# Kernel optimization log

Measured on AMD Instinct MI355X. Metric: run time of the kernel, lower is better.

The kernel has to match this reference:

```python
import jax, jax.numpy as jnp
import numpy as np

NUM_GRIDS = 8
GRID_MIN, GRID_MAX = -2.0, 2.0
DENOM = (GRID_MAX - GRID_MIN) / (NUM_GRIDS - 1)
GRID = jnp.linspace(GRID_MIN, GRID_MAX, NUM_GRIDS, dtype=jnp.float32)

Q_DIM = K_DIM = V_DIM = 256
HEAD_DIM, NUM_HEADS = 32, 8
TOTAL = HEAD_DIM * NUM_HEADS  # 256
B, S = 128, 8192


def fastkan(x, spline_w, base_w, base_b):
    # RBF expansion: [N, in, G] (layernorm in original is built but never applied)
    basis = jnp.exp(-(((x[..., None] - GRID) / DENOM) ** 2))
    ret = basis.reshape(x.shape[0], -1) @ spline_w          # [N, out]
    base = jax.nn.silu(x) @ base_w + base_b                 # [N, out]
    return ret + base


def setup_inputs() -> dict:
    key = jax.random.key(0)
    ks = jax.random.split(key, 20)
    d = {
        "q": jax.random.normal(ks[0], (B, Q_DIM), jnp.float32),
        "k": jax.random.normal(ks[1], (S, K_DIM), jnp.float32),
        "v": jax.random.normal(ks[2], (S, V_DIM), jnp.float32),
    }
    i = 3
    for name, din, dout in (("q", Q_DIM, TOTAL), ("k", K_DIM, TOTAL), ("v", V_DIM, TOTAL), ("g", Q_DIM, TOTAL), ("o", TOTAL, Q_DIM)):
        d[f"{name}_sw"] = jax.random.truncated_normal(ks[i], -2.0, 2.0, (din * NUM_GRIDS, dout), jnp.float32) * 0.1
        d[f"{name}_bw"] = jax.random.normal(ks[i + 1], (din, dout), jnp.float32) * (1.0 / np.sqrt(din))
        d[f"{name}_bb"] = jnp.zeros((dout,), jnp.float32)
        i += 2
    return d


def reference(q, k, v,
              q_sw, q_bw, q_bb,
              k_sw, k_bw, k_bb,
              v_sw, v_bw, v_bb,
              g_sw, g_bw, g_bb,
              o_sw, o_bw, o_bb):
    norm = 1.0 / np.sqrt(HEAD_DIM)
    wq = (fastkan(q, q_sw, q_bw, q_bb) * norm).reshape(B, NUM_HEADS, HEAD_DIM)   # [B,H,D]
    wk = fastkan(k, k_sw, k_bw, k_bb).reshape(S, NUM_HEADS, HEAD_DIM)            # [S,H,D]
    # broadcast-multiply + reduce == einsum; softmax over key axis S
    att = jax.nn.softmax(jnp.einsum("bhd,shd->bsh", wq, wk), axis=1)             # [B,S,H]
    wv = fastkan(v, v_sw, v_bw, v_bb).reshape(S, NUM_HEADS, HEAD_DIM)            # [S,H,D]
    o = jnp.einsum("bsh,shd->bhd", att, wv).reshape(B, TOTAL)                    # [B,H*D]
    g = jax.nn.sigmoid(fastkan(q, g_sw, g_bw, g_bb))                             # [B,H*D]
    o = g * o
    return fastkan(o, o_sw, o_bw, o_bb)                                          # [B,q_dim]
```

## Files before the change

kernel.cpp:

```cpp
#include <hip/hip_runtime.h>
#include <math.h>

#define IN_DIM 256
#define OUT_DIM 256

typedef short short8 __attribute__((ext_vector_type(8)));
typedef short short4_t __attribute__((ext_vector_type(4)));
typedef float f32x4 __attribute__((ext_vector_type(4)));
typedef unsigned int u32;

static __device__ __forceinline__ short f2bf(float f) {
    union { float f; unsigned u; } c; c.f = f;
    unsigned r = (c.u + 0x7FFFu + ((c.u >> 16) & 1u)) >> 16;
    return (short)r;
}
static __device__ __forceinline__ float bf2f(short s) {
    union { unsigned u; float f; } c;
    c.u = ((u32)(unsigned short)s) << 16;
    return c.f;
}

static __device__ __forceinline__ void gload16(const void* g, void* l) {
    __builtin_amdgcn_global_load_lds(
        (const __attribute__((address_space(1))) u32*)g,
        (__attribute__((address_space(3))) u32*)l, 16, 0, 0);
}

template<int RT, int CT, int MODE>
__global__ __launch_bounds__(256) void fastkan_kernel(
    const float* __restrict__ X, const float* __restrict__ SW,
    const float* __restrict__ BW, const float* __restrict__ BB,
    float* __restrict__ OUT)
{
    constexpr int TRT = RT / 16;
    constexpr int TCT = CT / 16;
    __shared__ float aT[64][RT];
    __shared__ float bT[64][CT];
    const int t = threadIdx.x, tr = t >> 4, tc = t & 15;
    const int r0 = blockIdx.x * RT, c0 = blockIdx.y * CT;
    float acc[TRT][TCT];
#pragma unroll
    for (int a = 0; a < TRT; ++a)
#pragma unroll
        for (int b = 0; b < TCT; ++b) acc[a][b] = 0.f;

    for (int i0 = 0; i0 < IN_DIM; i0 += 8) {
        __syncthreads();
        constexpr int PER_A = (RT * 8) / 256;
#pragma unroll
        for (int j = 0; j < PER_A; ++j) {
            int p = j * 256 + t;
            int i = p & 7, r = p >> 3;
            float x = X[(size_t)(r0 + r) * IN_DIM + (i0 + i)];
#pragma unroll
            for (int g = 0; g < 8; ++g) {
                float z = (x - (-2.0f + (float)g * (4.0f / 7.0f))) * 1.75f;
                aT[i * 8 + g][r] = __expf(-z * z);
            }
        }
#pragma unroll
        for (int j = 0; j < (64 * CT) / 1024; ++j) {
            int p = j * 256 + t;
            int c4 = p % (CT / 4), kk = p / (CT / 4);
            *(float4*)&bT[kk][c4 * 4] =
                *(const float4*)&SW[(size_t)(i0 * 8 + kk) * OUT_DIM + (c0 + c4 * 4)];
        }
        __syncthreads();
#pragma unroll 8
        for (int kk = 0; kk < 64; ++kk) {
            float av[TRT], bv[TCT];
#pragma unroll
            for (int a = 0; a < TRT; ++a) av[a] = aT[kk][tr * TRT + a];
#pragma unroll
            for (int b = 0; b < TCT; ++b) bv[b] = bT[kk][tc * TCT + b];
#pragma unroll
            for (int a = 0; a < TRT; ++a)
#pragma unroll
                for (int b = 0; b < TCT; ++b)
                    acc[a][b] = fmaf(av[a], bv[b], acc[a][b]);
        }
    }
    for (int i0 = 0; i0 < IN_DIM; i0 += 64) {
        __syncthreads();
#pragma unroll
        for (int j = 0; j < (RT * 64) / 1024; ++j) {
            int p = j * 256 + t;
            int i4 = p & 15, r = p >> 4;
            float4 xv = *(const float4*)&X[(size_t)(r0 + r) * IN_DIM + (i0 + i4 * 4)];
            const float* xe = &xv.x;
#pragma unroll
            for (int e = 0; e < 4; ++e) {
                float x = xe[e];
                aT[i4 * 4 + e][r] = x / (1.f + __expf(-x));
            }
        }
#pragma unroll
        for (int j = 0; j < (64 * CT) / 1024; ++j) {
            int p = j * 256 + t;
            int c4 = p % (CT / 4), kk = p / (CT / 4);
            *(float4*)&bT[kk][c4 * 4] =
                *(const float4*)&BW[(size_t)(i0 + kk) * OUT_DIM + (c0 + c4 * 4)];
        }
        __syncthreads();
#pragma unroll 8
        for (int kk = 0; kk < 64; ++kk) {
            float av[TRT], bv[TCT];
#pragma unroll
            for (int a = 0; a < TRT; ++a) av[a] = aT[kk][tr * TRT + a];
#pragma unroll
            for (int b = 0; b < TCT; ++b) bv[b] = bT[kk][tc * TCT + b];
#pragma unroll
            for (int a = 0; a < TRT; ++a)
#pragma unroll
                for (int b = 0; b < TCT; ++b)
                    acc[a][b] = fmaf(av[a], bv[b], acc[a][b]);
        }
    }
#pragma unroll
    for (int a = 0; a < TRT; ++a) {
        int r = r0 + tr * TRT + a;
#pragma unroll
        for (int b = 0; b < TCT; ++b) {
            int c = c0 + tc * TCT + b;
            float v = acc[a][b] + BB[c];
            if (MODE == 1) v *= 0.17677669529663687f;
            if (MODE == 2) v = 1.f / (1.f + __expf(-v));
            OUT[(size_t)r * OUT_DIM + c] = v;
        }
    }
}

__global__ __launch_bounds__(256) void fastkan_splitk(
    const float* __restrict__ X,
    const float* __restrict__ SW0, const float* __restrict__ BW0,
    const float* __restrict__ SW1, const float* __restrict__ BW1,
    float* __restrict__ PART)
{
    __shared__ float aT[128][65];
    __shared__ float bT[64][33];

    const int t = threadIdx.x;
    const int tr = t >> 4, tc = t & 15;
    const int c0 = blockIdx.x * 32;
    const int kc = blockIdx.y;
    const int z = blockIdx.z;
    const float* SW = z ? SW1 : SW0;
    const float* BW = z ? BW1 : BW0;

    float acc[8][2];
#pragma unroll
    for (int a = 0; a < 8; ++a) { acc[a][0] = 0.f; acc[a][1] = 0.f; }

    for (int sub = 0; sub < 4; ++sub) {
        const int k0 = kc * 256 + sub * 64;
        __syncthreads();
        if (kc < 8) {
            const int i0 = kc * 32 + sub * 8;
#pragma unroll
            for (int it = 0; it < 4; ++it) {
                int p = it * 256 + t;
                int row = p & 127, i = p >> 7;
                float x = X[(size_t)row * 256 + i0 + i];
#pragma unroll
                for (int g = 0; g < 8; ++g) {
                    float zz = (x - (-2.0f + (float)g * (4.0f / 7.0f))) * 1.75f;
                    aT[row][i * 8 + g] = __expf(-zz * zz);
                }
            }
        } else {
            const int f0 = sub * 64;
            int row = t >> 1, seg = t & 1;
            const float* xr = &X[(size_t)row * 256 + f0 + seg * 32];
#pragma unroll
            for (int j4 = 0; j4 < 8; ++j4) {
                float4 xv = *(const float4*)&xr[j4 * 4];
                const float* xe = &xv.x;
#pragma unroll
                for (int e = 0; e < 4; ++e) {
                    float x = xe[e];
                    aT[row][seg * 32 + j4 * 4 + e] = x / (1.f + __expf(-x));
                }
            }
        }
        {
            const float* Wsrc = (kc < 8) ? &SW[(size_t)k0 * 256] : &BW[(size_t)(k0 - 2048) * 256];
#pragma unroll
            for (int it = 0; it < 2; ++it) {
                int p = it * 256 + t;
                int kk = p >> 3, c4 = p & 7;
                float4 v = *(const float4*)&Wsrc[(size_t)kk * 256 + c0 + c4 * 4];
                bT[kk][c4 * 4 + 0] = v.x; bT[kk][c4 * 4 + 1] = v.y;
                bT[kk][c4 * 4 + 2] = v.z; bT[kk][c4 * 4 + 3] = v.w;
            }
        }
        __syncthreads();
#pragma unroll 8
        for (int kk = 0; kk < 64; ++kk) {
            float av[8], bv[2];
#pragma unroll
            for (int a = 0; a < 8; ++a) av[a] = aT[tr * 8 + a][kk];
            bv[0] = bT[kk][tc * 2 + 0];
            bv[1] = bT[kk][tc * 2 + 1];
#pragma unroll
            for (int a = 0; a < 8; ++a) {
                acc[a][0] = fmaf(av[a], bv[0], acc[a][0]);
                acc[a][1] = fmaf(av[a], bv[1], acc[a][1]);
            }
        }
    }
#pragma unroll
    for (int a = 0; a < 8; ++a) {
        int r = tr * 8 + a;
        float* dst = &PART[((size_t)(z * 9 + kc) * 128 + r) * 256 + c0 + tc * 2];
        dst[0] = acc[a][0];
        dst[1] = acc[a][1];
    }
}

template<int MODE>
__global__ __launch_bounds__(256) void reduce_kernel(
    const float* __restrict__ PART, const float* __restrict__ BB, float* __restrict__ OUT)
{
    const int r = blockIdx.x, t = threadIdx.x;
    float s = 0.f;
#pragma unroll
    for (int kc = 0; kc < 9; ++kc)
        s += PART[((size_t)kc * 128 + r) * 256 + t];
    float v = s + BB[t];
    if (MODE == 1) v *= 0.17677669529663687f;
    if (MODE == 2) v = 1.f / (1.f + __expf(-v));
    OUT[(size_t)r * 256 + t] = v;
}

template<int WB>
__global__ __launch_bounds__(256) void reduce_qg(
    const float* __restrict__ PART, const float* __restrict__ QBB,
    const float* __restrict__ GBB, float* __restrict__ WQ, float* __restrict__ GB,
    short* __restrict__ WQb)
{
    const int r = blockIdx.x, t = threadIdx.x, z = blockIdx.y;
    const float* P = PART + (size_t)z * 9 * 128 * 256;
    float s = 0.f;
#pragma unroll
    for (int kc = 0; kc < 9; ++kc)
        s += P[((size_t)kc * 128 + r) * 256 + t];
    if (z == 0) {
        float v = (s + QBB[t]) * 0.17677669529663687f;
        WQ[(size_t)r * 256 + t] = v;
        if (WB) WQb[(size_t)r * 256 + t] = f2bf(v);
    } else {
        float v = s + GBB[t];
        GB[(size_t)r * 256 + t] = 1.f / (1.f + __expf(-v));
    }
}

__global__ __launch_bounds__(256) void prep_kernel(
    const float* __restrict__ SWk, const float* __restrict__ BWk, short* __restrict__ Bk,
    const float* __restrict__ SWv, const float* __restrict__ BWv, short* __restrict__ Bv)
{
    __shared__ float tile[64][65];
    const int t = threadIdx.x;
    const int kk0 = blockIdx.x * 64;
    const int c0 = blockIdx.y * 64;
    const float* SW = blockIdx.z ? SWv : SWk;
    const float* BW = blockIdx.z ? BWv : BWk;
    short* Bdst = blockIdx.z ? Bv : Bk;

#pragma unroll
    for (int j = 0; j < 4; ++j) {
        int p = j * 256 + t;
        int lr = p >> 4, lc4 = p & 15;
        float4 v;
        if (kk0 < 2048) v = *(const float4*)&SW[(size_t)(kk0 + lr) * 256 + c0 + lc4 * 4];
        else            v = *(const float4*)&BW[(size_t)(kk0 - 2048 + lr) * 256 + c0 + lc4 * 4];
        tile[lr][lc4 * 4 + 0] = v.x; tile[lr][lc4 * 4 + 1] = v.y;
        tile[lr][lc4 * 4 + 2] = v.z; tile[lr][lc4 * 4 + 3] = v.w;
    }
    __syncthreads();
#pragma unroll
    for (int j = 0; j < 4; ++j) {
        int p = j * 256 + t;
        int lc = p >> 4, lk4 = p & 15;
        short4_t s;
#pragma unroll
        for (int e = 0; e < 4; ++e) s[e] = f2bf(tile[lk4 * 4 + e][lc]);
        *(short4_t*)&Bdst[(size_t)(c0 + lc) * 2304 + kk0 + lk4 * 4] = s;
    }
}

__global__ __launch_bounds__(256) void basis_gen2(
    const float* __restrict__ K, const float* __restrict__ V,
    short* __restrict__ A0, short* __restrict__ A1)
{
    const float* X = blockIdx.y ? V : K;
    short* A = blockIdx.y ? A1 : A0;
    const int row = blockIdx.x;
    const int t = threadIdx.x;
    float x = X[(size_t)row * 256 + t];
    short8 s;
#pragma unroll
    for (int g = 0; g < 8; ++g) {
        float z = (x - (-2.0f + (float)g * (4.0f / 7.0f))) * 1.75f;
        s[g] = f2bf(__expf(-z * z));
    }
    *(short8*)&A[(size_t)row * 2304 + t * 8] = s;
    if (t < 32) {
        const float* xr = &X[(size_t)row * 256 + t * 8];
        short8 sl;
#pragma unroll
        for (int e2 = 0; e2 < 2; ++e2) {
            float4 xv = *(const float4*)&xr[e2 * 4];
            const float* xe = &xv.x;
#pragma unroll
            for (int e = 0; e < 4; ++e) {
                float xx = xe[e];
                sl[e2 * 4 + e] = f2bf(xx / (1.f + __expf(-xx)));
            }
        }
        *(short8*)&A[(size_t)row * 2304 + 2048 + t * 8] = sl;
    }
}

__global__ __launch_bounds__(256) void prep_basis(
    const float* __restrict__ K, const float* __restrict__ V,
    short* __restrict__ A0, short* __restrict__ A1,
    const float* __restrict__ SWk, const float* __restrict__ BWk, short* __restrict__ Bk,
    const float* __restrict__ SWv, const float* __restrict__ BWv, short* __restrict__ Bv)
{
    __shared__ float tile[64][65];
    const int bid = blockIdx.x;
    const int t = threadIdx.x;
    if (bid < 16384) {
        const float* X = (bid >> 13) ? V : K;
        short* A = (bid >> 13) ? A1 : A0;
        const int row = bid & 8191;
        float x = X[(size_t)row * 256 + t];
        short8 s;
#pragma unroll
        for (int g = 0; g < 8; ++g) {
            float z = (x - (-2.0f + (float)g * (4.0f / 7.0f))) * 1.75f;
            s[g] = f2bf(__expf(-z * z));
        }
        *(short8*)&A[(size_t)row * 2304 + t * 8] = s;
        if (t < 32) {
            const float* xr = &X[(size_t)row * 256 + t * 8];
            short8 sl;
#pragma unroll
            for (int e2 = 0; e2 < 2; ++e2) {
                float4 xv = *(const float4*)&xr[e2 * 4];
                const float* xe = &xv.x;
#pragma unroll
                for (int e = 0; e < 4; ++e) {
                    float xx = xe[e];
                    sl[e2 * 4 + e] = f2bf(xx / (1.f + __expf(-xx)));
                }
            }
            *(short8*)&A[(size_t)row * 2304 + 2048 + t * 8] = sl;
        }
        return;
    }
    const int p = bid - 16384;
    const int zz = p / 144;
    const int q = p % 144;
    const int kk0 = (q >> 2) * 64;
    const int c0 = (q & 3) * 64;
    const float* SW = zz ? SWv : SWk;
    const float* BW = zz ? BWv : BWk;
    short* Bdst = zz ? Bv : Bk;

#pragma unroll
    for (int j = 0; j < 4; ++j) {
        int pp = j * 256 + t;
        int lr = pp >> 4, lc4 = pp & 15;
        float4 v;
        if (kk0 < 2048) v = *(const float4*)&SW[(size_t)(kk0 + lr) * 256 + c0 + lc4 * 4];
        else            v = *(const float4*)&BW[(size_t)(kk0 - 2048 + lr) * 256 + c0 + lc4 * 4];
        tile[lr][lc4 * 4 + 0] = v.x; tile[lr][lc4 * 4 + 1] = v.y;
        tile[lr][lc4 * 4 + 2] = v.z; tile[lr][lc4 * 4 + 3] = v.w;
    }
    __syncthreads();
#pragma unroll
    for (int j = 0; j < 4; ++j) {
        int pp = j * 256 + t;
        int lc = pp >> 4, lk4 = pp & 15;
        short4_t s;
#pragma unroll
        for (int e = 0; e < 4; ++e) s[e] = f2bf(tile[lk4 * 4 + e][lc]);
        *(short4_t*)&Bdst[(size_t)(c0 + lc) * 2304 + kk0 + lk4 * 4] = s;
    }
}

__global__ __launch_bounds__(256) void stage2(
    const short* __restrict__ A0, const short* __restrict__ A1,
    const short* __restrict__ Bk, const short* __restrict__ Bv,
    const float* __restrict__ BBk, const float* __restrict__ BBv,
    short* __restrict__ GPk0, short* __restrict__ GPk1,
    short* __restrict__ GPv0, short* __restrict__ GPv1,
    const float* __restrict__ PART, const float* __restrict__ QBB,
    const float* __restrict__ GBB, float* __restrict__ GB,
    short* __restrict__ WQb)
{
    __shared__ __align__(16) short Al[128 * 64];
    __shared__ __align__(16) short Bl[128 * 64];

    const int bid = blockIdx.x;
    const int t = threadIdx.x;

    if (bid >= 512) {
        const int p = bid - 512;
        const int r = p % 128, z = p / 128;
        const float* P = PART + (size_t)z * 9 * 128 * 256;
        float s = 0.f;
#pragma unroll
        for (int kc = 0; kc < 9; ++kc)
            s += P[((size_t)kc * 128 + r) * 256 + t];
        if (z == 0) {
            WQb[(size_t)r * 256 + t] = f2bf((s + QBB[t]) * 0.17677669529663687f);
        } else {
            float v = s + GBB[t];
            GB[(size_t)r * 256 + t] = 1.f / (1.f + __expf(-v));
        }
        return;
    }

    const int x = bid & 63;
    const int y = (bid >> 6) & 1;
    const int z = bid >> 7;
    const int mat = z >> 1, kh = z & 1;
    const short* A  = mat ? A1 : A0;
    const short* B2 = mat ? Bv : Bk;
    const float* BB = mat ? BBv : BBk;
    short* OUT = mat ? (kh ? GPv1 : GPv0) : (kh ? GPk1 : GPk0);

    const int r0 = x * 128;
    const int c0 = y * 128;
    const int kbase = kh * 1152;
    const int lane = t & 63, wid = t >> 6;
    const int wm = wid >> 1, wn = wid & 1;
    const int lrow = lane & 15;
    const int lkb = (lane >> 4) * 16;

    f32x4 acc[4][4];
#pragma unroll
    for (int a = 0; a < 4; ++a)
#pragma unroll
        for (int c = 0; c < 4; ++c) acc[a][c] = (f32x4){0.f, 0.f, 0.f, 0.f};

    for (int st = 0; st < 18; ++st) {
        const int k0 = kbase + st * 64;
        __syncthreads();
#pragma unroll
        for (int i = 0; i < 4; ++i) {
            int f = i * 256 + t;
            int row = f >> 3, kg = f & 7;
            gload16(&A[(size_t)(r0 + row) * 2304 + k0 + kg * 8], (char*)Al + f * 16);
        }
#pragma unroll
        for (int i = 0; i < 4; ++i) {
            int f = i * 256 + t;
            int c = f >> 3, kg = f & 7;
            gload16(&B2[(size_t)(c0 + c) * 2304 + k0 + kg * 8], (char*)Bl + f * 16);
        }
        __syncthreads();
#pragma unroll
        for (int kf = 0; kf < 2; ++kf) {
            short8 af[4], bf[4];
#pragma unroll
            for (int a = 0; a < 4; ++a) {
                int R = wm * 64 + a * 16 + lrow;
                af[a] = *(short8*)((char*)Al + R * 128 + kf * 64 + lkb);
            }
#pragma unroll
            for (int c = 0; c < 4; ++c) {
                int C = wn * 64 + c * 16 + lrow;
                bf[c] = *(short8*)((char*)Bl + C * 128 + kf * 64 + lkb);
            }
#pragma unroll
            for (int a = 0; a < 4; ++a)
#pragma unroll
                for (int c = 0; c < 4; ++c)
                    acc[a][c] = __builtin_amdgcn_mfma_f32_16x16x32_bf16(af[a], bf[c], acc[a][c], 0, 0, 0);
        }
    }
#pragma unroll
    for (int a = 0; a < 4; ++a)
#pragma unroll
        for (int c = 0; c < 4; ++c) {
            int col = c0 + wn * 64 + c * 16 + lrow;
            float bias = (kh == 0) ? BB[col] : 0.f;
#pragma unroll
            for (int j = 0; j < 4; ++j) {
                int row = r0 + wm * 64 + a * 16 + (lane >> 4) * 4 + j;
                OUT[(size_t)row * 256 + col] = f2bf(acc[a][c][j] + bias);
            }
        }
}

__global__ __launch_bounds__(256) void gemm_tile(
    const short* __restrict__ A, const short* __restrict__ B2,
    const float* __restrict__ BB, float* __restrict__ OUT)
{
    __shared__ __align__(16) short A_l[64 * 64];
    __shared__ __align__(16) short B_l[64 * 64];
    char* ab = (char*)A_l;
    char* bb = (char*)B_l;

    const int t = threadIdx.x;
    const int r0 = blockIdx.x * 64;
    const int c0 = blockIdx.y * 64;
    const int lane = t & 63;
    const int wid = t >> 6;
    const int wm = wid >> 1, wn = wid & 1;
    const int lrow = lane & 15;
    const int lkb = (lane >> 4) * 16;

    f32x4 acc[2][2];
#pragma unroll
    for (int a = 0; a < 2; ++a)
#pragma unroll
        for (int c = 0; c < 2; ++c) acc[a][c] = (f32x4){0.f, 0.f, 0.f, 0.f};

    for (int st = 0; st < 36; ++st) {
        const int k0 = st * 64;
        __syncthreads();
#pragma unroll
        for (int it = 0; it < 2; ++it) {
            int p = it * 256 + t;
            int row = p >> 3, kg = p & 7;
            short8 s = *(const short8*)&A[(size_t)(r0 + row) * 2304 + k0 + kg * 8];
            int off = (row * 128 + kg * 16) ^ ((row & 7) << 4);
            *(short8*)(ab + off) = s;
        }
#pragma unroll
        for (int it = 0; it < 2; ++it) {
            int p = it * 256 + t;
            int c = p >> 3, kg = p & 7;
            short8 s = *(const short8*)&B2[(size_t)(c0 + c) * 2304 + k0 + kg * 8];
            int off = (c * 128 + kg * 16) ^ ((c & 7) << 4);
            *(short8*)(bb + off) = s;
        }
        __syncthreads();
#pragma unroll
        for (int kf = 0; kf < 2; ++kf) {
            short8 af[2], bf[2];
#pragma unroll
            for (int a = 0; a < 2; ++a) {
                int R = wm * 32 + a * 16 + lrow;
                int off = (R * 128 + kf * 64 + lkb) ^ ((R & 7) << 4);
                af[a] = *(short8*)(ab + off);
            }
#pragma unroll
            for (int c = 0; c < 2; ++c) {
                int R = wn * 32 + c * 16 + lrow;
                int off = (R * 128 + kf * 64 + lkb) ^ ((R & 7) << 4);
                bf[c] = *(short8*)(bb + off);
            }
#pragma unroll
            for (int a = 0; a < 2; ++a)
#pragma unroll
                for (int c = 0; c < 2; ++c)
                    acc[a][c] = __builtin_amdgcn_mfma_f32_16x16x32_bf16(af[a], bf[c], acc[a][c], 0, 0, 0);
        }
    }
#pragma unroll
    for (int a = 0; a < 2; ++a)
#pragma unroll
        for (int c = 0; c < 2; ++c) {
            int col = c0 + wn * 32 + c * 16 + (lane & 15);
            float bias = BB[col];
#pragma unroll
            for (int j = 0; j < 4; ++j) {
                int row = r0 + wm * 32 + a * 16 + (lane >> 4) * 4 + j;
                OUT[(size_t)row * 256 + col] = acc[a][c][j] + bias;
            }
        }
}

__global__ __launch_bounds__(256) void attn_mfma(
    const short* __restrict__ WQb,
    const short* __restrict__ K0, const short* __restrict__ K1,
    const short* __restrict__ V0, const short* __restrict__ V1,
    float* __restrict__ OPART, float* __restrict__ LPART)
{
    __shared__ __align__(16) short Ql[128 * 32];
    __shared__ __align__(16) short Kl[64 * 32];
    __shared__ __align__(16) short Vt[32 * 64];
    __shared__ __align__(16) short El[128 * 64];
    char* ql = (char*)Ql; char* kl = (char*)Kl;
    char* vt = (char*)Vt; char* el = (char*)El;

    const int t = threadIdx.x, lane = t & 63, w = t >> 6;
    const int ch = blockIdx.x, h = blockIdx.y, s0 = ch * 64;
    const int lr = lane & 15, lg = lane >> 4;

    {
        int f = t;
        gload16(&WQb[(size_t)(f >> 2) * 256 + h * 32 + (f & 3) * 8], ql + f * 16);
        f = t + 256;
        gload16(&WQb[(size_t)(f >> 2) * 256 + h * 32 + (f & 3) * 8], ql + f * 16);
        int s = t >> 2, d8 = (t & 3) * 8;
        size_t off = (size_t)(s0 + s) * 256 + h * 32 + d8;
        short8 ka = *(const short8*)&K0[off];
        short8 kb = *(const short8*)&K1[off];
        short8 ks;
#pragma unroll
        for (int e = 0; e < 8; ++e) ks[e] = f2bf(bf2f(ka[e]) + bf2f(kb[e]));
        *(short8*)(kl + t * 16) = ks;
        short8 va = *(const short8*)&V0[off];
        short8 vb = *(const short8*)&V1[off];
#pragma unroll
        for (int e = 0; e < 8; ++e) {
            int d = d8 + e;
            *(short*)(vt + ((d * 128 + s * 2) ^ ((d & 7) << 4))) = f2bf(bf2f(va[e]) + bf2f(vb[e]));
        }
    }
    __syncthreads();

#pragma unroll
    for (int i = 0; i < 2; ++i) {
        const int q = (w * 2 + i) * 16 + lr;
        short8 bq = *(short8*)(ql + q * 64 + lg * 16);
        float ls = 0.f;
#pragma unroll
        for (int j = 0; j < 4; ++j) {
            short8 ak = *(short8*)(kl + (j * 16 + lr) * 64 + lg * 16);
            f32x4 sc = {0.f, 0.f, 0.f, 0.f};
            sc = __builtin_amdgcn_mfma_f32_16x16x32_bf16(ak, bq, sc, 0, 0, 0);
            short4_t ep;
#pragma unroll
            for (int jj = 0; jj < 4; ++jj) {
                float e = __expf(sc[jj] - 16.0f);
                ls += e;
                ep[jj] = f2bf(e);
            }
            int sb = j * 16 + lg * 4;
            *(short4_t*)(el + ((q * 128 + sb * 2) ^ ((q & 7) << 4))) = ep;
        }
        ls += __shfl_xor(ls, 16);
        ls += __shfl_xor(ls, 32);
        if (lg == 0)
            LPART[(size_t)(ch * 8 + h) * 128 + (w * 2 + i) * 16 + lr] = ls;
    }
    __syncthreads();

    f32x4 oacc[2][2];
#pragma unroll
    for (int i = 0; i < 2; ++i)
#pragma unroll
        for (int d = 0; d < 2; ++d) oacc[i][d] = (f32x4){0.f, 0.f, 0.f, 0.f};
#pragma unroll
    for (int kf = 0; kf < 2; ++kf) {
        short8 ea[2], vb[2];
#pragma unroll
        for (int i = 0; i < 2; ++i) {
            int q = (w * 2 + i) * 16 + lr;
            ea[i] = *(short8*)(el + ((q * 128 + kf * 64 + lg * 16) ^ ((q & 7) << 4)));
        }
#pragma unroll
        for (int d = 0; d < 2; ++d) {
            int dd = d * 16 + lr;
            vb[d] = *(short8*)(vt + ((dd * 128 + kf * 64 + lg * 16) ^ ((dd & 7) << 4)));
        }
#pragma unroll
        for (int i = 0; i < 2; ++i)
#pragma unroll
            for (int d = 0; d < 2; ++d)
                oacc[i][d] = __builtin_amdgcn_mfma_f32_16x16x32_bf16(ea[i], vb[d], oacc[i][d], 0, 0, 0);
    }
#pragma unroll
    for (int i = 0; i < 2; ++i)
#pragma unroll
        for (int d = 0; d < 2; ++d) {
            int dd = d * 16 + lr;
#pragma unroll
            for (int j = 0; j < 4; ++j) {
                int q = (w * 2 + i) * 16 + lg * 4 + j;
                OPART[((size_t)(ch * 8 + h) * 128 + q) * 32 + dd] = oacc[i][d][j];
            }
        }
}

__global__ __launch_bounds__(256) void attn_reduce2(
    const float* __restrict__ OPART, const float* __restrict__ LPART,
    const float* __restrict__ G, float* __restrict__ OMID)
{
    __shared__ float so[8][33];
    __shared__ float sl[8];
    const int b = blockIdx.x, h = blockIdx.y;
    const int t = threadIdx.x;
    const int d = t & 31, part = t >> 5;
    float o = 0.f, l = 0.f;
#pragma unroll 4
    for (int cc = 0; cc < 16; ++cc) {
        int ch = part * 16 + cc;
        o += OPART[((size_t)(ch * 8 + h) * 128 + b) * 32 + d];
        l += LPART[(size_t)(ch * 8 + h) * 128 + b];
    }
    so[part][d] = o;
    if (d == 0) sl[part] = l;
    __syncthreads();
    if (t < 32) {
        float oo = 0.f, ll = 0.f;
#pragma unroll
        for (int p = 0; p < 8; ++p) { oo += so[p][t]; ll += sl[p]; }
        int idx = b * 256 + h * 32 + t;
        OMID[idx] = G[idx] * (oo / ll);
    }
}

__global__ __launch_bounds__(256) void attn_chunk(
    const float* __restrict__ WQ, const float* __restrict__ WK, const float* __restrict__ WV,
    float* __restrict__ OPART, float* __restrict__ LPART)
{
    __shared__ float sWQ[128][33];
    __shared__ float sWK[64][33];
    __shared__ float sWV[64][33];
    __shared__ float sE[128][66];
    __shared__ float lred[128][16];

    const int t = threadIdx.x;
    const int ch = blockIdx.x;
    const int h = blockIdx.y;
    const int s0 = ch * 64;

    {
        int b = t >> 1, seg = t & 1;
        const float* src = &WQ[(size_t)b * 256 + h * 32 + seg * 16];
#pragma unroll
        for (int j = 0; j < 4; ++j) {
            float4 v = *(const float4*)&src[j * 4];
            sWQ[b][seg * 16 + j * 4 + 0] = v.x; sWQ[b][seg * 16 + j * 4 + 1] = v.y;
            sWQ[b][seg * 16 + j * 4 + 2] = v.z; sWQ[b][seg * 16 + j * 4 + 3] = v.w;
        }
        if (t < 128) {
            int s = t >> 1; seg = t & 1;
            const float* sk = &WK[(size_t)(s0 + s) * 256 + h * 32 + seg * 16];
#pragma unroll
            for (int j = 0; j < 4; ++j) {
                float4 v = *(const float4*)&sk[j * 4];
                sWK[s][seg * 16 + j * 4 + 0] = v.x; sWK[s][seg * 16 + j * 4 + 1] = v.y;
                sWK[s][seg * 16 + j * 4 + 2] = v.z; sWK[s][seg * 16 + j * 4 + 3] = v.w;
            }
        } else {
            int t2 = t - 128;
            int s = t2 >> 1; seg = t2 & 1;
            const float* sv = &WV[(size_t)(s0 + s) * 256 + h * 32 + seg * 16];
#pragma unroll
            for (int j = 0; j < 4; ++j) {
                float4 v = *(const float4*)&sv[j * 4];
                sWV[s][seg * 16 + j * 4 + 0] = v.x; sWV[s][seg * 16 + j * 4 + 1] = v.y;
                sWV[s][seg * 16 + j * 4 + 2] = v.z; sWV[s][seg * 16 + j * 4 + 3] = v.w;
            }
        }
    }
    __syncthreads();

    const int tr = t >> 4, tc = t & 15;
    {
        float acc[8][4];
#pragma unroll
        for (int a = 0; a < 8; ++a)
#pragma unroll
            for (int b = 0; b < 4; ++b) acc[a][b] = 0.f;
#pragma unroll 4
        for (int kk = 0; kk < 32; ++kk) {
            float av[8], bv[4];
#pragma unroll
            for (int a = 0; a < 8; ++a) av[a] = sWQ[tr * 8 + a][kk];
#pragma unroll
            for (int b = 0; b < 4; ++b) bv[b] = sWK[tc * 4 + b][kk];
#pragma unroll
            for (int a = 0; a < 8; ++a)
#pragma unroll
                for (int b = 0; b < 4; ++b) acc[a][b] = fmaf(av[a], bv[b], acc[a][b]);
        }
#pragma unroll
        for (int a = 0; a < 8; ++a) {
            float lp = 0.f;
#pragma unroll
            for (int b = 0; b < 4; ++b) {
                float e = __expf(acc[a][b] - 16.0f);
                sE[tr * 8 + a][tc * 4 + b] = e;
                lp += e;
            }
            lred[tr * 8 + a][tc] = lp;
        }
    }
    __syncthreads();
    if (t < 128) {
        float l = 0.f;
#pragma unroll
        for (int j = 0; j < 16; ++j) l += lred[t][j];
        LPART[(size_t)(ch * 8 + h) * 128 + t] = l;
    }

    {
        float acc2[8][2];
#pragma unroll
        for (int a = 0; a < 8; ++a) { acc2[a][0] = 0.f; acc2[a][1] = 0.f; }
#pragma unroll 4
        for (int kk = 0; kk < 64; ++kk) {
            float av[8], bv[2];
#pragma unroll
            for (int a = 0; a < 8; ++a) av[a] = sE[tr * 8 + a][kk];
            bv[0] = sWV[kk][tc * 2 + 0];
            bv[1] = sWV[kk][tc * 2 + 1];
#pragma unroll
            for (int a = 0; a < 8; ++a) {
                acc2[a][0] = fmaf(av[a], bv[0], acc2[a][0]);
                acc2[a][1] = fmaf(av[a], bv[1], acc2[a][1]);
            }
        }
#pragma unroll
        for (int a = 0; a < 8; ++a) {
            int b = tr * 8 + a;
            float* dst = &OPART[((size_t)(ch * 8 + h) * 128 + b) * 32 + tc * 2];
            dst[0] = acc2[a][0];
            dst[1] = acc2[a][1];
        }
    }
}

__global__ __launch_bounds__(256) void attn_reduce(
    const float* __restrict__ OPART, const float* __restrict__ LPART,
    const float* __restrict__ G, float* __restrict__ OMID)
{
    const int b = blockIdx.x;
    const int t = threadIdx.x;
    const int h = t >> 5, d = t & 31;
    float o = 0.f, l = 0.f;
    for (int ch = 0; ch < 128; ++ch) {
        o += OPART[((size_t)(ch * 8 + h) * 128 + b) * 32 + d];
        l += LPART[(size_t)(ch * 8 + h) * 128 + b];
    }
    int idx = b * 256 + h * 32 + d;
    OMID[idx] = G[idx] * (o / l);
}

__global__ __launch_bounds__(256) void attn_kernel(
    const float* __restrict__ WQ, const float* __restrict__ WK, const float* __restrict__ WV,
    const float* __restrict__ G, float* __restrict__ OMID)
{
    __shared__ float red[4][64][33];
    const int h = blockIdx.y;
    const int bl = threadIdx.x >> 6;
    const int lane = threadIdx.x & 63;
    const int b = blockIdx.x * 4 + bl;
    float q[32];
    {
        const float* wq = &WQ[(size_t)b * 256 + h * 32];
#pragma unroll
        for (int j = 0; j < 8; ++j) {
            float4 v = *(const float4*)&wq[j * 4];
            q[j * 4 + 0] = v.x; q[j * 4 + 1] = v.y; q[j * 4 + 2] = v.z; q[j * 4 + 3] = v.w;
        }
    }
    float o[32];
#pragma unroll
    for (int d = 0; d < 32; ++d) o[d] = 0.f;
    float l = 0.f;
#pragma unroll 2
    for (int s = lane; s < 8192; s += 64) {
        const float* kr = &WK[(size_t)s * 256 + h * 32];
        float s0 = 0, s1 = 0, s2 = 0, s3 = 0;
#pragma unroll
        for (int j = 0; j < 8; ++j) {
            float4 kv = *(const float4*)&kr[j * 4];
            s0 = fmaf(q[j * 4 + 0], kv.x, s0);
            s1 = fmaf(q[j * 4 + 1], kv.y, s1);
            s2 = fmaf(q[j * 4 + 2], kv.z, s2);
            s3 = fmaf(q[j * 4 + 3], kv.w, s3);
        }
        float e = __expf((s0 + s1) + (s2 + s3) - 16.0f);
        l += e;
        const float* vr = &WV[(size_t)s * 256 + h * 32];
#pragma unroll
        for (int j = 0; j < 8; ++j) {
            float4 vv = *(const float4*)&vr[j * 4];
            o[j * 4 + 0] = fmaf(e, vv.x, o[j * 4 + 0]);
            o[j * 4 + 1] = fmaf(e, vv.y, o[j * 4 + 1]);
            o[j * 4 + 2] = fmaf(e, vv.z, o[j * 4 + 2]);
            o[j * 4 + 3] = fmaf(e, vv.w, o[j * 4 + 3]);
        }
    }
#pragma unroll
    for (int d = 0; d < 32; ++d) red[bl][lane][d] = o[d];
    red[bl][lane][32] = l;
    __syncthreads();
    if (threadIdx.x < 128) {
        int bl2 = threadIdx.x >> 5;
        int d = threadIdx.x & 31;
        float os = 0.f, ls = 0.f;
#pragma unroll 8
        for (int ln = 0; ln < 64; ++ln) {
            os += red[bl2][ln][d];
            ls += red[bl2][ln][32];
        }
        int b2 = blockIdx.x * 4 + bl2;
        int idx = b2 * 256 + h * 32 + d;
        OMID[idx] = G[idx] * (os / ls);
    }
}

extern "C" void kernel_launch(void* const* d_in, const int* in_sizes, int n_in,
                              void* d_out, int out_size, void* d_ws, size_t ws_size,
                              hipStream_t stream) {
    const float* q    = (const float*)d_in[0];
    const float* k    = (const float*)d_in[1];
    const float* v    = (const float*)d_in[2];
    const float* q_sw = (const float*)d_in[3];
    const float* q_bw = (const float*)d_in[4];
    const float* q_bb = (const float*)d_in[5];
    const float* k_sw = (const float*)d_in[6];
    const float* k_bw = (const float*)d_in[7];
    const float* k_bb = (const float*)d_in[8];
    const float* v_sw = (const float*)d_in[9];
    const float* v_bw = (const float*)d_in[10];
    const float* v_bb = (const float*)d_in[11];
    const float* g_sw = (const float*)d_in[12];
    const float* g_bw = (const float*)d_in[13];
    const float* g_bb = (const float*)d_in[14];
    const float* o_sw = (const float*)d_in[15];
    const float* o_bw = (const float*)d_in[16];
    const float* o_bb = (const float*)d_in[17];

    float* ws = (float*)d_ws;
    float* wk = ws;
    float* wv = ws + 2097152;
    float* wq = ws + 4194304;
    float* gb = ws + 4227072;
    float* om = ws + 4259840;
    short* Bk = (short*)(ws + 4292608);
    short* Bv = (short*)(ws + 4587520);
    float* Opart = ws + 4882432;
    float* Lpart = ws + 9076736;
    float* PART = Opart;
    short* A0 = (short*)(ws + 9207808);
    short* A1 = (short*)(ws + 18644992);
    short* GPk0 = (short*)(ws + 28082176);
    short* GPk1 = (short*)(ws + 29130752);
    short* GPv0 = (short*)(ws + 30179328);
    short* GPv1 = (short*)(ws + 31227904);
    short* WQb  = (short*)(ws + 32276480);
    short* Abuf = (short*)Opart;
    float* out = (float*)d_out;

    const bool can_mfma   = ws_size >= (size_t)4882432 * 4;
    const bool can_bigger = ws_size >= (size_t)(4882432 + 9437184) * 4;
    const bool can_huge   = ws_size >= (size_t)32292864 * 4;

    dim3 blk(256);
    if (can_huge) {
        prep_basis<<<dim3(16672), blk, 0, stream>>>(k, v, A0, A1,
                                                    k_sw, k_bw, Bk, v_sw, v_bw, Bv);
        fastkan_splitk<<<dim3(8, 9, 2), blk, 0, stream>>>(q, q_sw, q_bw, g_sw, g_bw, PART);
        stage2<<<dim3(768), blk, 0, stream>>>(A0, A1, Bk, Bv, k_bb, v_bb,
                                              GPk0, GPk1, GPv0, GPv1,
                                              PART, q_bb, g_bb, gb, WQb);
        attn_mfma<<<dim3(128, 8), blk, 0, stream>>>(WQb, GPk0, GPk1, GPv0, GPv1, Opart, Lpart);
        attn_reduce2<<<dim3(128, 8), blk, 0, stream>>>(Opart, Lpart, gb, om);
        fastkan_splitk<<<dim3(8, 9, 1), blk, 0, stream>>>(om, o_sw, o_bw, o_sw, o_bw, PART);
        reduce_kernel<0><<<dim3(128), blk, 0, stream>>>(PART, o_bb, out);
    } else if (can_bigger) {
        prep_kernel<<<dim3(36, 4, 2), blk, 0, stream>>>(k_sw, k_bw, Bk, v_sw, v_bw, Bv);
        fastkan_splitk<<<dim3(8, 9, 2), blk, 0, stream>>>(q, q_sw, q_bw, g_sw, g_bw, PART);
        reduce_qg<0><<<dim3(128, 2), blk, 0, stream>>>(PART, q_bb, g_bb, wq, gb, (short*)wq);
        basis_gen2<<<dim3(8192, 1), blk, 0, stream>>>(k, k, Abuf, Abuf);
        gemm_tile<<<dim3(128, 4), blk, 0, stream>>>(Abuf, Bk, k_bb, wk);
        basis_gen2<<<dim3(8192, 1), blk, 0, stream>>>(v, v, Abuf, Abuf);
        gemm_tile<<<dim3(128, 4), blk, 0, stream>>>(Abuf, Bv, v_bb, wv);
        attn_chunk<<<dim3(128, 8), blk, 0, stream>>>(wq, wk, wv, Opart, Lpart);
        attn_reduce<<<dim3(128), blk, 0, stream>>>(Opart, Lpart, gb, om);
        fastkan_splitk<<<dim3(8, 9, 1), blk, 0, stream>>>(om, o_sw, o_bw, o_sw, o_bw, PART);
        reduce_kernel<0><<<dim3(128), blk, 0, stream>>>(PART, o_bb, out);
    } else {
        fastkan_kernel<64, 64, 0><<<dim3(128, 4), blk, 0, stream>>>(k, k_sw, k_bw, k_bb, wk);
        fastkan_kernel<64, 64, 0><<<dim3(128, 4), blk, 0, stream>>>(v, v_sw, v_bw, v_bb, wv);
        fastkan_kernel<32, 32, 1><<<dim3(4, 8), blk, 0, stream>>>(q, q_sw, q_bw, q_bb, wq);
        fastkan_kernel<32, 32, 2><<<dim3(4, 8), blk, 0, stream>>>(q, g_sw, g_bw, g_bb, gb);
        attn_kernel<<<dim3(32, 8), blk, 0, stream>>>(wq, wk, wv, gb, om);
        fastkan_kernel<32, 32, 0><<<dim3(4, 8), blk, 0, stream>>>(om, o_sw, o_bw, o_bb, out);
    }
}
```

Before: 113.0 us.

## Fold q/g FastKAN projections into prep_basis and stage2 bf16 MFMA GEMM

```diff
diff --git a/kernel.cpp b/kernel.cpp
--- a/kernel.cpp
+++ b/kernel.cpp
@@ -322,17 +322,20 @@
 }
 
 __global__ __launch_bounds__(256) void prep_basis(
-    const float* __restrict__ K, const float* __restrict__ V,
-    short* __restrict__ A0, short* __restrict__ A1,
+    const float* __restrict__ K, const float* __restrict__ V, const float* __restrict__ Q,
+    short* __restrict__ A0, short* __restrict__ A1, short* __restrict__ Aq,
     const float* __restrict__ SWk, const float* __restrict__ BWk, short* __restrict__ Bk,
-    const float* __restrict__ SWv, const float* __restrict__ BWv, short* __restrict__ Bv)
+    const float* __restrict__ SWv, const float* __restrict__ BWv, short* __restrict__ Bv,
+    const float* __restrict__ SWq, const float* __restrict__ BWq, short* __restrict__ Bq,
+    const float* __restrict__ SWg, const float* __restrict__ BWg, short* __restrict__ Bg)
 {
     __shared__ float tile[64][65];
     const int bid = blockIdx.x;
     const int t = threadIdx.x;
-    if (bid < 16384) {
-        const float* X = (bid >> 13) ? V : K;
-        short* A = (bid >> 13) ? A1 : A0;
+    if (bid < 16512) {
+        const int m = bid >> 13;
+        const float* X = (m == 0) ? K : ((m == 1) ? V : Q);
+        short* A = (m == 0) ? A0 : ((m == 1) ? A1 : Aq);
         const int row = bid & 8191;
         float x = X[(size_t)row * 256 + t];
         short8 s;
@@ -359,14 +362,14 @@
         }
         return;
     }
-    const int p = bid - 16384;
-    const int zz = p / 144;
+    const int p = bid - 16512;
+    const int mat = p / 144;
     const int q = p % 144;
     const int kk0 = (q >> 2) * 64;
     const int c0 = (q & 3) * 64;
-    const float* SW = zz ? SWv : SWk;
-    const float* BW = zz ? BWv : BWk;
-    short* Bdst = zz ? Bv : Bk;
+    const float* SW = (mat == 0) ? SWk : ((mat == 1) ? SWv : ((mat == 2) ? SWq : SWg));
+    const float* BW = (mat == 0) ? BWk : ((mat == 1) ? BWv : ((mat == 2) ? BWq : BWg));
+    short* Bdst     = (mat == 0) ? Bk  : ((mat == 1) ? Bv  : ((mat == 2) ? Bq  : Bg));
 
 #pragma unroll
     for (int j = 0; j < 4; ++j) {
@@ -391,62 +394,50 @@
 }
 
 __global__ __launch_bounds__(256) void stage2(
-    const short* __restrict__ A0, const short* __restrict__ A1,
+    const short* __restrict__ A0, const short* __restrict__ A1, const short* __restrict__ Aq,
     const short* __restrict__ Bk, const short* __restrict__ Bv,
+    const short* __restrict__ Bq, const short* __restrict__ Bg,
     const float* __restrict__ BBk, const float* __restrict__ BBv,
+    const float* __restrict__ QBB, const float* __restrict__ GBB,
     short* __restrict__ GPk0, short* __restrict__ GPk1,
     short* __restrict__ GPv0, short* __restrict__ GPv1,
-    const float* __restrict__ PART, const float* __restrict__ QBB,
-    const float* __restrict__ GBB, float* __restrict__ GB,
-    short* __restrict__ WQb)
+    short* __restrict__ WQb, float* __restrict__ GB)
 {
     __shared__ __align__(16) short Al[128 * 64];
     __shared__ __align__(16) short Bl[128 * 64];
 
     const int bid = blockIdx.x;
     const int t = threadIdx.x;
-
-    if (bid >= 512) {
-        const int p = bid - 512;
-        const int r = p % 128, z = p / 128;
-        const float* P = PART + (size_t)z * 9 * 128 * 256;
-        float s = 0.f;
-#pragma unroll
-        for (int kc = 0; kc < 9; ++kc)
-            s += P[((size_t)kc * 128 + r) * 256 + t];
-        if (z == 0) {
-            WQb[(size_t)r * 256 + t] = f2bf((s + QBB[t]) * 0.17677669529663687f);
-        } else {
-            float v = s + GBB[t];
-            GB[(size_t)r * 256 + t] = 1.f / (1.f + __expf(-v));
-        }
-        return;
-    }
-
-    const int x = bid & 63;
-    const int y = (bid >> 6) & 1;
-    const int z = bid >> 7;
-    const int mat = z >> 1, kh = z & 1;
-    const short* A  = mat ? A1 : A0;
-    const short* B2 = mat ? Bv : Bk;
-    const float* BB = mat ? BBv : BBk;
-    short* OUT = mat ? (kh ? GPv1 : GPv0) : (kh ? GPk1 : GPk0);
-
-    const int r0 = x * 128;
-    const int c0 = y * 128;
-    const int kbase = kh * 1152;
     const int lane = t & 63, wid = t >> 6;
     const int wm = wid >> 1, wn = wid & 1;
     const int lrow = lane & 15;
     const int lkb = (lane >> 4) * 16;
 
+    const short* A;
+    const short* B2;
+    int r0, c0, kbase, nst;
+    if (bid < 4) {
+        A = Aq;
+        B2 = (bid >> 1) ? Bg : Bq;
+        r0 = 0; c0 = (bid & 1) * 128;
+        kbase = 0; nst = 36;
+    } else {
+        const int b4 = bid - 4;
+        const int z = b4 >> 7;
+        A  = (z >> 1) ? A1 : A0;
+        B2 = (z >> 1) ? Bv : Bk;
+        r0 = (b4 & 63) * 128;
+        c0 = ((b4 >> 6) & 1) * 128;
+        kbase = (z & 1) * 1152; nst = 18;
+    }
+
     f32x4 acc[4][4];
 #pragma unroll
     for (int a = 0; a < 4; ++a)
 #pragma unroll
         for (int c = 0; c < 4; ++c) acc[a][c] = (f32x4){0.f, 0.f, 0.f, 0.f};
 
-    for (int st = 0; st < 18; ++st) {
+    for (int st = 0; st < nst; ++st) {
         const int k0 = kbase + st * 64;
         __syncthreads();
 #pragma unroll
@@ -482,6 +473,34 @@
                     acc[a][c] = __builtin_amdgcn_mfma_f32_16x16x32_bf16(af[a], bf[c], acc[a][c], 0, 0, 0);
         }
     }
+
+    if (bid < 4) {
+        const int l = bid >> 1;
+#pragma unroll
+        for (int a = 0; a < 4; ++a)
+#pragma unroll
+            for (int c = 0; c < 4; ++c) {
+                int col = c0 + wn * 64 + c * 16 + lrow;
+#pragma unroll
+                for (int j = 0; j < 4; ++j) {
+                    int row = wm * 64 + a * 16 + (lane >> 4) * 4 + j;
+                    if (l == 0) {
+                        WQb[(size_t)row * 256 + col] =
+                            f2bf((acc[a][c][j] + QBB[col]) * 0.17677669529663687f);
+                    } else {
+                        float v = acc[a][c][j] + GBB[col];
+                        GB[(size_t)row * 256 + col] = 1.f / (1.f + __expf(-v));
+                    }
+                }
+            }
+        return;
+    }
+
+    const int b4 = bid - 4;
+    const int z = b4 >> 7;
+    const int mat = z >> 1, kh = z & 1;
+    const float* BB = mat ? BBv : BBk;
+    short* OUT = mat ? (kh ? GPv1 : GPv0) : (kh ? GPk1 : GPk0);
 #pragma unroll
     for (int a = 0; a < 4; ++a)
 #pragma unroll
@@ -942,21 +961,25 @@
     short* GPv0 = (short*)(ws + 30179328);
     short* GPv1 = (short*)(ws + 31227904);
     short* WQb  = (short*)(ws + 32276480);
+    short* Bq   = (short*)(ws + 32292864);
+    short* Bg   = (short*)(ws + 32587776);
+    short* Aq   = (short*)(ws + 32882688);
     short* Abuf = (short*)Opart;
     float* out = (float*)d_out;
 
     const bool can_mfma   = ws_size >= (size_t)4882432 * 4;
     const bool can_bigger = ws_size >= (size_t)(4882432 + 9437184) * 4;
-    const bool can_huge   = ws_size >= (size_t)32292864 * 4;
+    const bool can_huge   = ws_size >= (size_t)32956416 * 4;
 
     dim3 blk(256);
     if (can_huge) {
-        prep_basis<<<dim3(16672), blk, 0, stream>>>(k, v, A0, A1,
-                                                    k_sw, k_bw, Bk, v_sw, v_bw, Bv);
-        fastkan_splitk<<<dim3(8, 9, 2), blk, 0, stream>>>(q, q_sw, q_bw, g_sw, g_bw, PART);
-        stage2<<<dim3(768), blk, 0, stream>>>(A0, A1, Bk, Bv, k_bb, v_bb,
-                                              GPk0, GPk1, GPv0, GPv1,
-                                              PART, q_bb, g_bb, gb, WQb);
+        prep_basis<<<dim3(17088), blk, 0, stream>>>(
+            k, v, q, A0, A1, Aq,
+            k_sw, k_bw, Bk, v_sw, v_bw, Bv,
+            q_sw, q_bw, Bq, g_sw, g_bw, Bg);
+        stage2<<<dim3(516), blk, 0, stream>>>(
+            A0, A1, Aq, Bk, Bv, Bq, Bg, k_bb, v_bb, q_bb, g_bb,
+            GPk0, GPk1, GPv0, GPv1, WQb, gb);
         attn_mfma<<<dim3(128, 8), blk, 0, stream>>>(WQb, GPk0, GPk1, GPv0, GPv1, Opart, Lpart);
         attn_reduce2<<<dim3(128, 8), blk, 0, stream>>>(Opart, Lpart, gb, om);
         fastkan_splitk<<<dim3(8, 9, 1), blk, 0, stream>>>(om, o_sw, o_bw, o_sw, o_bw, PART);
```

Measured after the change: 124.4 us. 10.2% more time.
